# Kernel optimization log

Hardware: AMD Instinct MI355X
Metric: run time of the kernel (lower is better)

Reference implementation:

```python
import jax, jax.numpy as jnp
import numpy as np

TEMPERATURE = 0.1
NEG_INF = -9e15

def setup_inputs() -> dict:
    key = jax.random.key(0)
    k1, k2 = jax.random.split(key)
    B, D = 4096, 256
    z_i = jax.random.normal(k1, (B, D), dtype=jnp.float32)
    z_j = jax.random.normal(k2, (B, D), dtype=jnp.float32)
    return {"z_i": z_i, "z_j": z_j}

def _l2norm(x, eps=1e-12):
    # matches F.normalize(dim=1): x / max(||x||, eps)
    n = jnp.sqrt(jnp.sum(x * x, axis=1, keepdims=True))
    return x / jnp.maximum(n, eps)

def reference(z_i, z_j):
    B = z_i.shape[0]
    zi = _l2norm(z_i)
    zj = _l2norm(z_j)
    reps = jnp.concatenate([zi, zj], axis=0)  # [2B, D], unit rows
    # cosine similarity of unit vectors == dot product
    sim = reps @ reps.T  # [2B, 2B]
    N = 2 * B
    eye = jnp.eye(N, dtype=bool)
    sim = jnp.where(eye, NEG_INF, sim)
    # positives: offset +B and -B diagonals
    pos = jnp.concatenate([sim[jnp.arange(B), jnp.arange(B) + B],
                           sim[jnp.arange(B) + B, jnp.arange(B)]], axis=0)  # [2B]
    pos = pos / TEMPERATURE
    sim = sim / TEMPERATURE
    denom = jnp.sum(jnp.exp(sim), axis=1)  # [2B]
    loss = -jnp.mean(pos - jnp.log(denom))
    return loss
```

## Files before the change

kernel.cpp:

```cpp
#include <hip/hip_runtime.h>
#include <hip/hip_bf16.h>
#include <stdint.h>

#define NROWS 8192
#define BROWS 4096
#define LN2 0.6931471805599453f
#define FSC 8.944507e-4f
#define NBLK 544

typedef __attribute__((ext_vector_type(4))) int i32x4;

__device__ inline void gload_lds16(const void* g, void* l) {
  __builtin_amdgcn_global_load_lds((const __attribute__((address_space(1))) void*)g,
                                   (__attribute__((address_space(3))) void*)l,
                                   16, 0, 0);
}

__global__ __launch_bounds__(256) void knorm(const float* __restrict__ zi,
                                             const float* __restrict__ zj,
                                             int* __restrict__ reps,
                                             float* __restrict__ denom,
                                             float* __restrict__ out) {
  int w = threadIdx.x >> 6, l = threadIdx.x & 63;
  int row = blockIdx.x * 4 + w;
  const float* src = (row < BROWS) ? (zi + (size_t)row * 256)
                                   : (zj + (size_t)(row - BROWS) * 256);
  float4 v = ((const float4*)src)[l];
  float ss = v.x * v.x + v.y * v.y + v.z * v.z + v.w * v.w;
#pragma unroll
  for (int m = 1; m < 64; m <<= 1) ss += __shfl_xor(ss, m, 64);
  float sc = 127.0f / fmaxf(sqrtf(ss), 1e-12f);
  int q0 = __float2int_rn(v.x * sc), q1 = __float2int_rn(v.y * sc);
  int q2 = __float2int_rn(v.z * sc), q3 = __float2int_rn(v.w * sc);
  reps[(size_t)row * 64 + l] =
      (q0 & 255) | ((q1 & 255) << 8) | ((q2 & 255) << 16) | ((q3 & 255) << 24);
  if (l == 0) denom[row] = 0.f;
  if (row == 0 && l == 0) out[0] = 0.f;
}

__global__ __launch_bounds__(256, 4) void ksim(const int* __restrict__ reps_,
                                               float* __restrict__ denom,
                                               float* __restrict__ pos) {
  __shared__ uint4 smem[2][1024];
  __shared__ float colacc[512];
  int tid = threadIdx.x, w = tid >> 6, l = tid & 63;
  int kgrp = l >> 4;

  int b = blockIdx.x;
  int orig = (b & 7) * 68 + (b >> 3);
  int rem = orig, it = 0, ch;
  while (rem >= (ch = (64 - it + 3) >> 2)) { rem -= ch; ++it; }
  int q = rem;
  int rowbase = it * 128;
  int cs0 = rowbase + q * 512;
  int len = NROWS - cs0; if (len > 512) len = 512;
  int ntile = len >> 6;

  colacc[tid] = 0.f; colacc[tid + 256] = 0.f;

  auto stage = [&](int bufi, int colbase) {
#pragma unroll
    for (int i = 0; i < 4; ++i) {
      int c2 = w * 4 + i;
      int lr = c2 * 4 + (l >> 4);
      int kb = ((l & 15) * 16) ^ ((lr & 3) << 4);
      gload_lds16((const char*)reps_ + (size_t)(colbase + lr) * 256 + kb,
                  (void*)&smem[bufi][c2 * 64]);
    }
  };
  stage(0, cs0);

  i32x4 a[2][4];
  {
    const uint4* r4 = (const uint4*)reps_;
    int arow = rowbase + w * 32 + (l & 15);
#pragma unroll
    for (int fr = 0; fr < 2; ++fr)
#pragma unroll
      for (int kk = 0; kk < 4; ++kk)
        a[fr][kk] = __builtin_bit_cast(i32x4,
            r4[(size_t)(arow + fr * 16) * 16 + kk * 4 + kgrp]);
  }

  int lds_a[4];
  {
    int r0l = l & 15;
    int swz = (r0l & 3) << 4;
#pragma unroll
    for (int kk = 0; kk < 4; ++kk)
      lds_a[kk] = r0l * 256 + ((kk * 64 + kgrp * 16) ^ swz);
  }

  float rowsum[2][4];
#pragma unroll
  for (int fr = 0; fr < 2; ++fr)
#pragma unroll
    for (int r = 0; r < 4; ++r) rowsum[fr][r] = 0.f;

  int r0 = rowbase + w * 32 + kgrp * 4;
  int buf = 0;

  for (int t = 0; t < ntile; ++t) {
    asm volatile("s_waitcnt vmcnt(0)" ::: "memory");
    __builtin_amdgcn_sched_barrier(0);
    __builtin_amdgcn_s_barrier();
    __builtin_amdgcn_sched_barrier(0);
    if (t + 1 < ntile) stage(buf ^ 1, cs0 + 64 * (t + 1));

    const char* bb = (const char*)&smem[0][0] + buf * 16384;
    i32x4 acc[2][4];
    const i32x4 zero = {0, 0, 0, 0};
    __builtin_amdgcn_s_setprio(1);
#pragma unroll
    for (int kk = 0; kk < 4; ++kk) {
      i32x4 bf[4];
#pragma unroll
      for (int fc = 0; fc < 4; ++fc)
        bf[fc] = *(const i32x4*)(bb + lds_a[kk] + fc * 4096);
#pragma unroll
      for (int fr = 0; fr < 2; ++fr)
#pragma unroll
        for (int fc = 0; fc < 4; ++fc) {
          if (kk == 0)
            acc[fr][fc] = __builtin_amdgcn_mfma_i32_16x16x64_i8(a[fr][0], bf[fc], zero, 0, 0, 0);
          else
            acc[fr][fc] = __builtin_amdgcn_mfma_i32_16x16x64_i8(a[fr][kk], bf[fc], acc[fr][fc], 0, 0, 0);
        }
    }
    __builtin_amdgcn_s_setprio(0);

    int cb = cs0 + 64 * t;
    bool docol = !(q == 0 && t < 2);
    bool dopos = (q == 8) && (t < 2) && (it < 32);
    float cp[4] = {0.f, 0.f, 0.f, 0.f};
    int cbase = cb + (l & 15);
#pragma unroll
    for (int fr = 0; fr < 2; ++fr)
#pragma unroll
      for (int fc = 0; fc < 4; ++fc)
#pragma unroll
        for (int r = 0; r < 4; ++r) {
          int rg = r0 + fr * 16 + r;
          int cg = cbase + fc * 16;
          float s = (float)acc[fr][fc][r] * FSC;
          float e = __builtin_amdgcn_exp2f(s);
          e = (rg == cg) ? 0.f : e;
          if (dopos && cg == rg + BROWS) pos[rg] = s;
          rowsum[fr][r] += e;
          cp[fc] += e;
        }
    if (docol) {
#pragma unroll
      for (int fc = 0; fc < 4; ++fc) {
        cp[fc] += __shfl_xor(cp[fc], 16, 64);
        cp[fc] += __shfl_xor(cp[fc], 32, 64);
      }
      if (l < 16) {
        int off = (cb - cs0) + l;
#pragma unroll
        for (int fc = 0; fc < 4; ++fc)
          atomicAdd(&colacc[off + fc * 16], cp[fc]);
      }
    }
    buf ^= 1;
  }

#pragma unroll
  for (int fr = 0; fr < 2; ++fr)
#pragma unroll
    for (int r = 0; r < 4; ++r) {
      float v = rowsum[fr][r];
      v += __shfl_xor(v, 1, 64);
      v += __shfl_xor(v, 2, 64);
      v += __shfl_xor(v, 4, 64);
      v += __shfl_xor(v, 8, 64);
      if ((l & 15) == 0) atomicAdd(&denom[r0 + fr * 16 + r], v);
    }

  __syncthreads();
#pragma unroll
  for (int i = 0; i < 2; ++i) {
    int off = tid + 256 * i;
    float v = colacc[off];
    int col = cs0 + off;
    if (col < NROWS && v != 0.f) atomicAdd(&denom[col], v);
  }
}

__global__ __launch_bounds__(256) void kfin(const float* __restrict__ denom,
                                            const float* __restrict__ pos,
                                            float* __restrict__ out) {
  int i = blockIdx.x * 256 + threadIdx.x;
  float v = (logf(denom[i]) - pos[i & 4095] * LN2) * (1.0f / 8192.0f);
#pragma unroll
  for (int m = 1; m < 64; m <<= 1) v += __shfl_xor(v, m, 64);
  __shared__ float part[4];
  if ((threadIdx.x & 63) == 0) part[threadIdx.x >> 6] = v;
  __syncthreads();
  if (threadIdx.x == 0)
    atomicAdd(out, part[0] + part[1] + part[2] + part[3]);
}

extern "C" void kernel_launch(void* const* d_in, const int* in_sizes, int n_in,
                              void* d_out, int out_size, void* d_ws, size_t ws_size,
                              hipStream_t stream) {
  (void)in_sizes; (void)n_in; (void)out_size; (void)ws_size;
  const float* zi = (const float*)d_in[0];
  const float* zj = (const float*)d_in[1];
  float* out = (float*)d_out;
  char* ws = (char*)d_ws;
  int* reps    = (int*)ws;
  float* denom = (float*)(ws + 2097152);
  float* pos   = (float*)(ws + 2097152 + 32768);

  knorm<<<2048, 256, 0, stream>>>(zi, zj, reps, denom, out);
  ksim<<<NBLK, 256, 0, stream>>>(reps, denom, pos);
  kfin<<<32, 256, 0, stream>>>(denom, pos, out);
}
```

Measured before the change: 42.45 us.

## Restructure similarity kernel into single-wave blocks with 64x32 tiles and no barriers

The similarity kernel moves from 4-wave blocks of 128-row strips to single-wave blocks that each own a 64-row strip and stream 32-column tiles. This doubles the block count and drops workgroup barriers and LDS atomics for column sums, since one wave owns the shared tile. The next tile's prefetch is issued before waiting, using a partial vmcnt, and the LDS swizzle is widened to 16 rows. In exchange, each column tile is reused by fewer rows, so global/L2 traffic per MFMA rises, and row-sum atomics to global memory double.

```diff
diff --git a/kernel.cpp b/kernel.cpp
--- a/kernel.cpp
+++ b/kernel.cpp
@@ -6,7 +6,7 @@
 #define BROWS 4096
 #define LN2 0.6931471805599453f
 #define FSC 8.944507e-4f
-#define NBLK 544
+#define NBLK 1088
 
 typedef __attribute__((ext_vector_type(4))) int i32x4;
 
@@ -38,89 +38,84 @@
   if (row == 0 && l == 0) out[0] = 0.f;
 }
 
-__global__ __launch_bounds__(256, 4) void ksim(const int* __restrict__ reps_,
-                                               float* __restrict__ denom,
-                                               float* __restrict__ pos) {
-  __shared__ uint4 smem[2][1024];
+__global__ __launch_bounds__(64, 2) void ksim(const int* __restrict__ reps_,
+                                              float* __restrict__ denom,
+                                              float* __restrict__ pos) {
+  __shared__ uint4 smem[2][512];
   __shared__ float colacc[512];
-  int tid = threadIdx.x, w = tid >> 6, l = tid & 63;
+  int l = threadIdx.x;
   int kgrp = l >> 4;
 
   int b = blockIdx.x;
-  int orig = (b & 7) * 68 + (b >> 3);
+  int orig = (b & 7) * 136 + (b >> 3);
   int rem = orig, it = 0, ch;
-  while (rem >= (ch = (64 - it + 3) >> 2)) { rem -= ch; ++it; }
+  while (rem >= (ch = (128 - it + 7) >> 3)) { rem -= ch; ++it; }
   int q = rem;
-  int rowbase = it * 128;
+  int rowbase = it * 64;
   int cs0 = rowbase + q * 512;
   int len = NROWS - cs0; if (len > 512) len = 512;
-  int ntile = len >> 6;
-
-  colacc[tid] = 0.f; colacc[tid + 256] = 0.f;
+  int ntile = len >> 5;
+
+#pragma unroll
+  for (int i = 0; i < 8; ++i) colacc[l + 64 * i] = 0.f;
 
   auto stage = [&](int bufi, int colbase) {
 #pragma unroll
-    for (int i = 0; i < 4; ++i) {
-      int c2 = w * 4 + i;
-      int lr = c2 * 4 + (l >> 4);
-      int kb = ((l & 15) * 16) ^ ((lr & 3) << 4);
+    for (int i = 0; i < 8; ++i) {
+      int lr = i * 4 + (l >> 4);
+      int kb = ((l & 15) * 16) ^ ((lr & 15) << 4);
       gload_lds16((const char*)reps_ + (size_t)(colbase + lr) * 256 + kb,
-                  (void*)&smem[bufi][c2 * 64]);
+                  (void*)&smem[bufi][i * 64]);
     }
   };
   stage(0, cs0);
 
-  i32x4 a[2][4];
+  i32x4 a[4][4];
   {
     const uint4* r4 = (const uint4*)reps_;
-    int arow = rowbase + w * 32 + (l & 15);
-#pragma unroll
-    for (int fr = 0; fr < 2; ++fr)
+    int arow = rowbase + (l & 15);
+#pragma unroll
+    for (int fr = 0; fr < 4; ++fr)
 #pragma unroll
       for (int kk = 0; kk < 4; ++kk)
         a[fr][kk] = __builtin_bit_cast(i32x4,
             r4[(size_t)(arow + fr * 16) * 16 + kk * 4 + kgrp]);
   }
 
-  int lds_a[4];
-  {
-    int r0l = l & 15;
-    int swz = (r0l & 3) << 4;
-#pragma unroll
-    for (int kk = 0; kk < 4; ++kk)
-      lds_a[kk] = r0l * 256 + ((kk * 64 + kgrp * 16) ^ swz);
-  }
-
-  float rowsum[2][4];
-#pragma unroll
-  for (int fr = 0; fr < 2; ++fr)
+  float rowsum[4][4];
+#pragma unroll
+  for (int fr = 0; fr < 4; ++fr)
 #pragma unroll
     for (int r = 0; r < 4; ++r) rowsum[fr][r] = 0.f;
 
-  int r0 = rowbase + w * 32 + kgrp * 4;
+  int r0 = rowbase + kgrp * 4;
   int buf = 0;
 
   for (int t = 0; t < ntile; ++t) {
-    asm volatile("s_waitcnt vmcnt(0)" ::: "memory");
+    if (t + 1 < ntile) {
+      stage(buf ^ 1, cs0 + 32 * (t + 1));
+      asm volatile("s_waitcnt vmcnt(8)" ::: "memory");
+    } else {
+      asm volatile("s_waitcnt vmcnt(0)" ::: "memory");
+    }
     __builtin_amdgcn_sched_barrier(0);
-    __builtin_amdgcn_s_barrier();
-    __builtin_amdgcn_sched_barrier(0);
-    if (t + 1 < ntile) stage(buf ^ 1, cs0 + 64 * (t + 1));
-
-    const char* bb = (const char*)&smem[0][0] + buf * 16384;
-    i32x4 acc[2][4];
+
+    const char* bb = (const char*)&smem[0][0] + buf * 8192;
+    i32x4 acc[4][2];
     const i32x4 zero = {0, 0, 0, 0};
     __builtin_amdgcn_s_setprio(1);
 #pragma unroll
     for (int kk = 0; kk < 4; ++kk) {
-      i32x4 bf[4];
-#pragma unroll
-      for (int fc = 0; fc < 4; ++fc)
-        bf[fc] = *(const i32x4*)(bb + lds_a[kk] + fc * 4096);
-#pragma unroll
-      for (int fr = 0; fr < 2; ++fr)
-#pragma unroll
-        for (int fc = 0; fc < 4; ++fc) {
+      i32x4 bf[2];
+#pragma unroll
+      for (int fc = 0; fc < 2; ++fc) {
+        int lr = (l & 15) + fc * 16;
+        bf[fc] = *(const i32x4*)(bb + lr * 256 + ((((kk * 4 + kgrp) ^ (lr & 15))) << 4));
+      }
+#pragma unroll
+      for (int fr = 0; fr < 4; ++fr)
+#pragma unroll
+        for (int fc = 0; fc < 2; ++fc) {
           if (kk == 0)
             acc[fr][fc] = __builtin_amdgcn_mfma_i32_16x16x64_i8(a[fr][0], bf[fc], zero, 0, 0, 0);
           else
@@ -129,15 +124,15 @@
     }
     __builtin_amdgcn_s_setprio(0);
 
-    int cb = cs0 + 64 * t;
+    int cb = cs0 + 32 * t;
     bool docol = !(q == 0 && t < 2);
-    bool dopos = (q == 8) && (t < 2) && (it < 32);
-    float cp[4] = {0.f, 0.f, 0.f, 0.f};
+    bool dopos = (q == 8) && (t < 2) && (it < 64);
+    float cp0 = 0.f, cp1 = 0.f;
     int cbase = cb + (l & 15);
 #pragma unroll
-    for (int fr = 0; fr < 2; ++fr)
-#pragma unroll
-      for (int fc = 0; fc < 4; ++fc)
+    for (int fr = 0; fr < 4; ++fr)
+#pragma unroll
+      for (int fc = 0; fc < 2; ++fc)
 #pragma unroll
         for (int r = 0; r < 4; ++r) {
           int rg = r0 + fr * 16 + r;
@@ -147,26 +142,22 @@
           e = (rg == cg) ? 0.f : e;
           if (dopos && cg == rg + BROWS) pos[rg] = s;
           rowsum[fr][r] += e;
-          cp[fc] += e;
+          if (fc == 0) cp0 += e; else cp1 += e;
         }
     if (docol) {
-#pragma unroll
-      for (int fc = 0; fc < 4; ++fc) {
-        cp[fc] += __shfl_xor(cp[fc], 16, 64);
-        cp[fc] += __shfl_xor(cp[fc], 32, 64);
-      }
+      cp0 += __shfl_xor(cp0, 16, 64); cp0 += __shfl_xor(cp0, 32, 64);
+      cp1 += __shfl_xor(cp1, 16, 64); cp1 += __shfl_xor(cp1, 32, 64);
       if (l < 16) {
         int off = (cb - cs0) + l;
-#pragma unroll
-        for (int fc = 0; fc < 4; ++fc)
-          atomicAdd(&colacc[off + fc * 16], cp[fc]);
+        colacc[off] += cp0;
+        colacc[off + 16] += cp1;
       }
     }
     buf ^= 1;
   }
 
 #pragma unroll
-  for (int fr = 0; fr < 2; ++fr)
+  for (int fr = 0; fr < 4; ++fr)
 #pragma unroll
     for (int r = 0; r < 4; ++r) {
       float v = rowsum[fr][r];
@@ -177,10 +168,9 @@
       if ((l & 15) == 0) atomicAdd(&denom[r0 + fr * 16 + r], v);
     }
 
-  __syncthreads();
-#pragma unroll
-  for (int i = 0; i < 2; ++i) {
-    int off = tid + 256 * i;
+#pragma unroll
+  for (int i = 0; i < 8; ++i) {
+    int off = l + 64 * i;
     float v = colacc[off];
     int col = cs0 + off;
     if (col < NROWS && v != 0.f) atomicAdd(&denom[col], v);
@@ -214,6 +204,6 @@
   float* pos   = (float*)(ws + 2097152 + 32768);
 
   knorm<<<2048, 256, 0, stream>>>(zi, zj, reps, denom, out);
-  ksim<<<NBLK, 256, 0, stream>>>(reps, denom, pos);
+  ksim<<<NBLK, 64, 0, stream>>>(reps, denom, pos);
   kfin<<<32, 256, 0, stream>>>(denom, pos, out);
 }
```

Measured after the change: 51.49 us. 21.3% more time.
